# Kernel tuning notes

Measured on AMD Instinct MI355X. Metric: run time of the kernel, lower is better.

## Reference

```python
import jax, jax.numpy as jnp
import numpy as np

N_REGS, R_BIT, N_OPS, FLIP = 8, 16, 16, 2

def bit2dec(bits):
    # little-endian soft bits -> decimal: sum_k b_k * 2^k
    k = jnp.arange(bits.shape[-1], dtype=bits.dtype)
    return jnp.sum(bits * jnp.exp2(k), axis=-1)

def addr_w(idx, n):
    # differentiable soft one-hot over n slots (linear interpolation kernel)
    grid = jnp.arange(n, dtype=idx.dtype)
    return jnp.maximum(1.0 - jnp.abs(idx[..., None] - grid), 0.0)

def setup_inputs():
    key = jax.random.key(0)
    ks = jax.random.split(key, 12)
    B, H, I, L = 8192, 512, 1024, 16
    return dict(
        z_hidden=jax.random.normal(ks[0], (B, H), jnp.float32),
        P_op=jax.random.uniform(ks[1], (B, L, 4), dtype=jnp.float32),
        P_dst=jax.random.uniform(ks[2], (B, L, 3), dtype=jnp.float32),
        P_src1=jax.random.uniform(ks[3], (B, L, 3), dtype=jnp.float32),
        P_src2=jax.random.uniform(ks[4], (B, L, 3), dtype=jnp.float32),
        P_imm=jax.random.uniform(ks[5], (B, L, 3), dtype=jnp.float32),
        Proglen=jax.random.uniform(ks[6], (B, 4), dtype=jnp.float32),
        group_num=16,
        W1=jax.random.normal(ks[7], (H, I), jnp.float32) / np.sqrt(H).astype(np.float32),
        b1=jnp.zeros((I,), jnp.float32),
        WR=jax.random.normal(ks[8], (I, N_REGS * R_BIT), jnp.float32) / np.sqrt(I).astype(np.float32),
        bR=jnp.zeros((N_REGS * R_BIT,), jnp.float32),
        Wt=jax.random.normal(ks[9], (I, 1), jnp.float32) / np.sqrt(I).astype(np.float32),
        bt=jnp.zeros((1,), jnp.float32),
        W_r2h=jax.random.normal(ks[10], (N_REGS, H), jnp.float32) / np.sqrt(N_REGS).astype(np.float32),
        b_r2h=jnp.zeros((H,), jnp.float32),
        ln_g=jnp.ones((H,), jnp.float32),
        ln_b=jnp.zeros((H,), jnp.float32),
    )

def reference(z_hidden, P_op, P_dst, P_src1, P_src2, P_imm, Proglen, group_num,
              W1, b1, WR, bR, Wt, bt, W_r2h, b_r2h, ln_g, ln_b):
    B, L, G = z_hidden.shape[0], P_op.shape[1], group_num
    # ---- Augmentation_Layer: MLP head -> R soft-bits + threshold ----
    h = jax.nn.relu(z_hidden @ W1 + b1)
    R_bits = jax.nn.sigmoid(h @ WR + bR).reshape(B, N_REGS, R_BIT)
    threshold = jax.nn.sigmoid(h @ Wt + bt)                 # [B,1]
    # ---- GroupSample.generate4R: flip FLIP random R-bits per candidate (cand 0 = original) ----
    idx = jax.random.randint(jax.random.key(42), (B, G, FLIP), 0, N_REGS * R_BIT)
    mask = jnp.clip(jax.nn.one_hot(idx, N_REGS * R_BIT, dtype=jnp.float32).sum(-2), 0.0, 1.0)
    mask = mask.at[:, 0].set(0.0).reshape(B, G, N_REGS, R_BIT)
    Rb = R_bits[:, None]                                    # [B,1,n_regs,r_bit]
    R = bit2dec(Rb + mask * (1.0 - 2.0 * Rb))               # [B,G,n_regs] decimals
    M = jnp.zeros_like(R)
    prog_len = jnp.broadcast_to(bit2dec(Proglen)[:, None], (B, G))
    dec = lambda x: bit2dec(x).T                            # [L,B]
    prog = (dec(P_op), dec(P_dst), dec(P_src1), dec(P_src2), dec(P_imm),
            jnp.arange(L, dtype=jnp.float32))

    # ---- MultiInterpreter: differentiable soft register machine ----
    def step(carry, xs):
        R, M = carry
        op_t, dst_t, s1_t, s2_t, imm_t, t = xs
        bc = lambda v: jnp.broadcast_to(v[:, None], (B, G))
        op_t, dst_t, s1_t, s2_t, imm_t = map(bc, (op_t, dst_t, s1_t, s2_t, imm_t))
        active = jnp.clip(prog_len - t, 0.0, 1.0)           # halt mask [B,G]
        w_d = addr_w(dst_t, N_REGS)                         # [B,G,n_regs]
        w_1 = addr_w(s1_t, N_REGS)
        w_2 = addr_w(s2_t, N_REGS)
        w_op = addr_w(op_t, N_OPS)                          # [B,G,16]
        r1 = jnp.sum(w_1 * R, -1); r2 = jnp.sum(w_2 * R, -1)
        m1 = jnp.sum(w_1 * M, -1); old = jnp.sum(w_d * R, -1)
        results = jnp.stack([
            old,                       # 0 NOP
            r1 + r2,                   # 1 ADD
            r1 - r2,                   # 2 SUB
            r1 * r2 / 65536.0,         # 3 MUL (scaled by 2^r_bit)
            r1,                        # 4 MOV
            imm_t,                     # 5 LOADI
            r1 + imm_t,                # 6 ADDI
            jnp.maximum(r1, r2),       # 7 MAX
            jnp.minimum(r1, r2),       # 8 MIN
            -r1,                       # 9 NEG
            0.5 * r1,                  # 10 SHR
            r2,                        # 11 MOV2
            m1,                        # 12 LOAD M[src1]
            old,                       # 13 STORE (reg unchanged)
            jnp.abs(r1),               # 14 ABS
            old,                       # 15 NOP
        ], axis=-1)
        res = jnp.sum(w_op * results, -1)                   # [B,G]
        p_store = w_op[..., 13]
        R = R + active[..., None] * w_d * (res[..., None] - R)
        M = M + (active * p_store)[..., None] * w_d * (r1[..., None] - M)
        return (R, M), None

    (R, M), _ = jax.lax.scan(step, (R, M), prog)
    # ---- register2hidden + LayerNorm ----
    reg_hidden = R @ W_r2h + b_r2h                          # [B,G,H]
    mu = reg_hidden.mean(-1, keepdims=True)
    var = reg_hidden.var(-1, keepdims=True)
    reg_hidden = (reg_hidden - mu) * jax.lax.rsqrt(var + 1e-5) * ln_g + ln_b
    return reg_hidden, threshold
```

## Files before the change

kernel.cpp:

```cpp
#include <hip/hip_runtime.h>
#include <stdint.h>

typedef __attribute__((ext_vector_type(8))) short short8;
typedef __attribute__((ext_vector_type(4))) float f32x4;
typedef __attribute__((ext_vector_type(8))) unsigned short ushort8;
typedef __attribute__((ext_vector_type(4))) unsigned short ushort4v;

__device__ __forceinline__ unsigned short f2bf(float f) {
  uint32_t u = __float_as_uint(f);
  uint32_t r = (u + 0x7fffu + ((u >> 16) & 1u)) >> 16;
  return (unsigned short)r;
}
__device__ __forceinline__ float bf2f(unsigned short v) {
  return __uint_as_float(((uint32_t)v) << 16);
}

typedef __attribute__((address_space(1))) const unsigned int g_u32;
typedef __attribute__((address_space(3))) unsigned int l_u32;
__device__ __forceinline__ void gl_lds16(const void* g, void* l) {
  __builtin_amdgcn_global_load_lds((g_u32*)g, (l_u32*)l, 16, 0, 0);
}

__device__ __forceinline__ uint32_t rotl32(uint32_t v, int d) { return (v << d) | (v >> (32 - d)); }

__device__ __forceinline__ void threefry2x32(uint32_t k0, uint32_t k1, uint32_t& x0, uint32_t& x1) {
  const uint32_t ks2 = k0 ^ k1 ^ 0x1BD11BDAu;
  x0 += k0; x1 += k1;
  x0 += x1; x1 = rotl32(x1, 13); x1 ^= x0;
  x0 += x1; x1 = rotl32(x1, 15); x1 ^= x0;
  x0 += x1; x1 = rotl32(x1, 26); x1 ^= x0;
  x0 += x1; x1 = rotl32(x1, 6);  x1 ^= x0;
  x0 += k1; x1 += ks2 + 1u;
  x0 += x1; x1 = rotl32(x1, 17); x1 ^= x0;
  x0 += x1; x1 = rotl32(x1, 29); x1 ^= x0;
  x0 += x1; x1 = rotl32(x1, 16); x1 ^= x0;
  x0 += x1; x1 = rotl32(x1, 24); x1 ^= x0;
  x0 += ks2; x1 += k0 + 2u;
  x0 += x1; x1 = rotl32(x1, 13); x1 ^= x0;
  x0 += x1; x1 = rotl32(x1, 15); x1 ^= x0;
  x0 += x1; x1 = rotl32(x1, 26); x1 ^= x0;
  x0 += x1; x1 = rotl32(x1, 6);  x1 ^= x0;
  x0 += k0; x1 += k1 + 3u;
  x0 += x1; x1 = rotl32(x1, 17); x1 ^= x0;
  x0 += x1; x1 = rotl32(x1, 29); x1 ^= x0;
  x0 += x1; x1 = rotl32(x1, 16); x1 ^= x0;
  x0 += x1; x1 = rotl32(x1, 24); x1 ^= x0;
  x0 += k1; x1 += ks2 + 4u;
  x0 += x1; x1 = rotl32(x1, 13); x1 ^= x0;
  x0 += x1; x1 = rotl32(x1, 15); x1 ^= x0;
  x0 += x1; x1 = rotl32(x1, 26); x1 ^= x0;
  x0 += x1; x1 = rotl32(x1, 6);  x1 ^= x0;
  x0 += ks2; x1 += k0 + 5u;
}

__global__ __launch_bounds__(256) void prep_kernel(const float* __restrict__ z,
                                                   unsigned short* __restrict__ zb, int n8,
                                                   const float* __restrict__ W1,
                                                   const float* __restrict__ WR,
                                                   unsigned short* __restrict__ W1t,
                                                   unsigned short* __restrict__ WRt,
                                                   const float* __restrict__ P_op,
                                                   const float* __restrict__ P_dst,
                                                   const float* __restrict__ P_s1,
                                                   const float* __restrict__ P_s2,
                                                   const float* __restrict__ P_imm,
                                                   const float* __restrict__ Plen,
                                                   float* __restrict__ prog,
                                                   float* __restrict__ plen, int BT) {
  __shared__ float t[32][33];
  const int tid = threadIdx.x;
  const int bx = blockIdx.x;
  if (bx < 2048) {
    const int i = bx * 256 + tid;
    if (i >= n8) return;
    const float4 a = reinterpret_cast<const float4*>(z)[i * 2];
    const float4 b = reinterpret_cast<const float4*>(z)[i * 2 + 1];
    ushort8 u;
    u[0] = f2bf(a.x); u[1] = f2bf(a.y); u[2] = f2bf(a.z); u[3] = f2bf(a.w);
    u[4] = f2bf(b.x); u[5] = f2bf(b.y); u[6] = f2bf(b.z); u[7] = f2bf(b.w);
    reinterpret_cast<ushort8*>(zb)[i] = u;
  } else if (bx < 2688) {
    const int b = bx - 2048;
    const float* src; unsigned short* dst; int N, K, k0, n0;
    if (b < 512) {
      src = W1; dst = W1t; N = 1024; K = 512;
      k0 = (b & 15) * 32; n0 = (b >> 4) * 32;
    } else {
      const int b2 = b - 512;
      src = WR; dst = WRt; N = 128; K = 1024;
      k0 = (b2 & 31) * 32; n0 = (b2 >> 5) * 32;
    }
    {
      const int row = tid >> 3, c4 = (tid & 7) * 4;
      const float4 v = *reinterpret_cast<const float4*>(&src[(size_t)(k0 + row) * N + n0 + c4]);
      t[row][c4] = v.x; t[row][c4 + 1] = v.y; t[row][c4 + 2] = v.z; t[row][c4 + 3] = v.w;
    }
    __syncthreads();
    {
      const int n = tid >> 3, k4 = (tid & 7) * 4;
      ushort4v o;
      o.x = f2bf(t[k4 + 0][n]); o.y = f2bf(t[k4 + 1][n]);
      o.z = f2bf(t[k4 + 2][n]); o.w = f2bf(t[k4 + 3][n]);
      *reinterpret_cast<ushort4v*>(&dst[(size_t)(n0 + n) * K + k0 + k4]) = o;
    }
  } else {
    const int i = (bx - 2688) * 256 + tid;
    if (i >= BT) return;
    const float* po = P_op + (size_t)i * 4;
    const float op = po[0] + 2.f * po[1] + 4.f * po[2] + 8.f * po[3];
    const float* pd = P_dst + (size_t)i * 3;
    const float dv = pd[0] + 2.f * pd[1] + 4.f * pd[2];
    const float* p1 = P_s1 + (size_t)i * 3;
    const float s1v = p1[0] + 2.f * p1[1] + 4.f * p1[2];
    const float* p2 = P_s2 + (size_t)i * 3;
    const float s2v = p2[0] + 2.f * p2[1] + 4.f * p2[2];
    const float* pi = P_imm + (size_t)i * 3;
    const float imv = pi[0] + 2.f * pi[1] + 4.f * pi[2];
    float* o = prog + (size_t)i * 5;
    o[0] = op; o[1] = dv; o[2] = s1v; o[3] = s2v; o[4] = imv;
    if ((i & 15) == 0) {
      const int b = i >> 4;
      const float* pl = Plen + (size_t)b * 4;
      plen[b] = pl[0] + 2.f * pl[1] + 4.f * pl[2] + 8.f * pl[3];
    }
  }
}

__global__ __launch_bounds__(256) void gemm_fused(const unsigned short* __restrict__ zb,
                                                  const unsigned short* __restrict__ W1t,
                                                  const float* __restrict__ b1,
                                                  const unsigned short* __restrict__ WRt,
                                                  const float* __restrict__ Wt,
                                                  float* __restrict__ part,
                                                  float* __restrict__ thr_part, int B) {
  __shared__ __align__(16) char smem[34816];
  unsigned short* AsF = (unsigned short*)smem;
  unsigned short* BsF = (unsigned short*)(smem + 16384);
  auto H2 = reinterpret_cast<unsigned short (*)[136]>(smem);

  const int tid = threadIdx.x;
  const int lane = tid & 63, wave = tid >> 6;
  const int wm = wave >> 1, wn = wave & 1;
  const int bx = blockIdx.x, bm = blockIdx.y * 128, bn = bx * 128;

  f32x4 acc[4][4];
#pragma unroll
  for (int i = 0; i < 4; ++i)
#pragma unroll
    for (int j = 0; j < 4; ++j) acc[i][j] = (f32x4)0.f;

  const int fr = lane & 15, kc = (lane >> 4) * 8;
  const int lr = (lane >> 4) * 4, lc = lane & 15;
  const int lrow = lane >> 3, slot = lane & 7;
  const int sslot = (slot ^ lrow) << 3;
  const int fx = fr & 7;
  const int cbase = lane >> 4;

  for (int k0 = 0; k0 < 512; k0 += 64) {
#pragma unroll
    for (int i = 0; i < 4; ++i) {
      const int r0 = wave * 32 + i * 8;
      gl_lds16(&zb[(size_t)(bm + r0 + lrow) * 512 + k0 + sslot], &AsF[r0 * 64]);
    }
#pragma unroll
    for (int i = 0; i < 4; ++i) {
      const int r0 = wave * 32 + i * 8;
      gl_lds16(&W1t[(size_t)(bn + r0 + lrow) * 512 + k0 + sslot], &BsF[r0 * 64]);
    }
    __syncthreads();
#pragma unroll
    for (int s = 0; s < 2; ++s) {
      short8 af[4], bfv[4];
#pragma unroll
      for (int f = 0; f < 4; ++f) {
        const int row = wm * 64 + f * 16 + fr;
        const int c = s * 4 + cbase;
        af[f] = *reinterpret_cast<const short8*>(&AsF[row * 64 + ((c ^ fx) << 3)]);
      }
#pragma unroll
      for (int f = 0; f < 4; ++f) {
        const int row = wn * 64 + f * 16 + fr;
        const int c = s * 4 + cbase;
        bfv[f] = *reinterpret_cast<const short8*>(&BsF[row * 64 + ((c ^ fx) << 3)]);
      }
#pragma unroll
      for (int fm = 0; fm < 4; ++fm)
#pragma unroll
        for (int fn = 0; fn < 4; ++fn)
          acc[fm][fn] = __builtin_amdgcn_mfma_f32_16x16x32_bf16(af[fm], bfv[fn], acc[fm][fn], 0, 0, 0);
    }
    __syncthreads();
  }

#pragma unroll
  for (int fn = 0; fn < 4; ++fn) {
    const int col_l = wn * 64 + fn * 16 + lc;
    const float bv = b1[bn + col_l];
#pragma unroll
    for (int fm = 0; fm < 4; ++fm) {
      const int row_l0 = wm * 64 + fm * 16 + lr;
#pragma unroll
      for (int r = 0; r < 4; ++r)
        H2[row_l0 + r][col_l] = f2bf(fmaxf(acc[fm][fn][r] + bv, 0.f));
    }
  }
  __syncthreads();

  {
    const int row = tid >> 1, half = tid & 1;
    const unsigned short* hp = &H2[row][half * 64];
    const float* wp = &Wt[bn + half * 64];
    float s = 0.f;
#pragma unroll
    for (int j = 0; j < 8; ++j) {
      const ushort8 a = *reinterpret_cast<const ushort8*>(hp + j * 8);
      const float4 w0 = *reinterpret_cast<const float4*>(wp + j * 8);
      const float4 w1 = *reinterpret_cast<const float4*>(wp + j * 8 + 4);
      s += bf2f(a[0]) * w0.x + bf2f(a[1]) * w0.y + bf2f(a[2]) * w0.z + bf2f(a[3]) * w0.w;
      s += bf2f(a[4]) * w1.x + bf2f(a[5]) * w1.y + bf2f(a[6]) * w1.z + bf2f(a[7]) * w1.w;
    }
    s += __shfl_xor(s, 1);
    if (half == 0) thr_part[(size_t)bx * B + bm + row] = s;
  }

  f32x4 acc2[4][4];
#pragma unroll
  for (int i = 0; i < 4; ++i)
#pragma unroll
    for (int j = 0; j < 4; ++j) acc2[i][j] = (f32x4)0.f;

#pragma unroll
  for (int ks = 0; ks < 4; ++ks) {
    short8 af2[4], bf2v[4];
#pragma unroll
    for (int fm = 0; fm < 4; ++fm)
      af2[fm] = *reinterpret_cast<const short8*>(&H2[wm * 64 + fm * 16 + fr][ks * 32 + kc]);
#pragma unroll
    for (int fn = 0; fn < 4; ++fn)
      bf2v[fn] = *reinterpret_cast<const short8*>(
          &WRt[(size_t)(wn * 64 + fn * 16 + fr) * 1024 + bn + ks * 32 + kc]);
#pragma unroll
    for (int fm = 0; fm < 4; ++fm)
#pragma unroll
      for (int fn = 0; fn < 4; ++fn)
        acc2[fm][fn] = __builtin_amdgcn_mfma_f32_16x16x32_bf16(af2[fm], bf2v[fn], acc2[fm][fn], 0, 0, 0);
  }

  float* pp = part + (size_t)bx * B * 128;
#pragma unroll
  for (int fn = 0; fn < 4; ++fn) {
    const int col = wn * 64 + fn * 16 + lc;
#pragma unroll
    for (int fm = 0; fm < 4; ++fm) {
      const int row0 = bm + wm * 64 + fm * 16 + lr;
#pragma unroll
      for (int r = 0; r < 4; ++r)
        pp[(size_t)(row0 + r) * 128 + col] = acc2[fm][fn][r];
    }
  }
}

__global__ __launch_bounds__(256) void scan2_kernel(const float* __restrict__ part,
                                                    const float* __restrict__ bR,
                                                    const float* __restrict__ thr_part,
                                                    const float* __restrict__ bt,
                                                    const float* __restrict__ prog,
                                                    const float* __restrict__ plen,
                                                    float* __restrict__ Rfinal,
                                                    float* __restrict__ thr_out, int B) {
  __shared__ float s_bits[16][128];
  __shared__ float s_prog[16][80];
  __shared__ float s_plen[16];
  const int tid = threadIdx.x;
  const int b0 = blockIdx.x * 16;
#pragma unroll
  for (int j = 0; j < 8; ++j) {
    const int f = tid + 256 * j;
    const int lb = f >> 7, c = f & 127;
    float s = part[(size_t)(b0 + lb) * 128 + c];
#pragma unroll
    for (int sl = 1; sl < 8; ++sl)
      s += part[(size_t)sl * B * 128 + (size_t)(b0 + lb) * 128 + c];
    s_bits[lb][c] = 1.f / (1.f + expf(-(s + bR[c])));
  }
#pragma unroll
  for (int j = 0; j < 5; ++j) {
    const int f = tid + 256 * j;
    s_prog[f / 80][f % 80] = prog[(size_t)b0 * 80 + f];
  }
  if (tid < 16) {
    s_plen[tid] = plen[b0 + tid];
    float s = thr_part[b0 + tid];
#pragma unroll
    for (int sl = 1; sl < 8; ++sl) s += thr_part[(size_t)sl * B + b0 + tid];
    thr_out[b0 + tid] = 1.f / (1.f + expf(-(s + bt[0])));
  }
  __syncthreads();

  const int lb = tid >> 4, g = tid & 15;
  const int bg = (b0 + lb) * 16 + g;

  uint32_t k2a, k2b;
  { uint32_t x0 = 0u, x1 = 1u; threefry2x32(0u, 42u, x0, x1); k2a = x0; k2b = x1; }
  uint32_t p0, p1;
  {
    uint32_t x0 = 0u, x1 = (uint32_t)bg * 2u;
    threefry2x32(k2a, k2b, x0, x1);
    p0 = (x0 ^ x1) & 127u;
  }
  {
    uint32_t x0 = 0u, x1 = (uint32_t)bg * 2u + 1u;
    threefry2x32(k2a, k2b, x0, x1);
    p1 = (x0 ^ x1) & 127u;
  }

  float R[8], M[8];
#pragma unroll
  for (int r = 0; r < 8; ++r) {
    float a = 0.f;
#pragma unroll
    for (int bit = 0; bit < 16; ++bit) {
      const int pos = r * 16 + bit;
      float v = s_bits[lb][pos];
      const bool flip = (g != 0) && ((int)p0 == pos || (int)p1 == pos);
      v = flip ? 1.0f - v : v;
      a = fmaf(v, (float)(1 << bit), a);
    }
    R[r] = a;
    M[r] = 0.f;
  }

  const float pl = s_plen[lb];
  for (int t = 0; t < 16; ++t) {
    const float op = s_prog[lb][t * 5 + 0];
    const float dst = s_prog[lb][t * 5 + 1];
    const float sa = s_prog[lb][t * 5 + 2];
    const float sb = s_prog[lb][t * 5 + 3];
    const float imm = s_prog[lb][t * 5 + 4];
    const float active = fminf(fmaxf(pl - (float)t, 0.f), 1.f);
    float r1 = 0.f, r2 = 0.f, m1 = 0.f, old = 0.f;
    float wd[8];
#pragma unroll
    for (int i = 0; i < 8; ++i) {
      const float w1 = fmaxf(1.f - fabsf(sa - (float)i), 0.f);
      const float w2 = fmaxf(1.f - fabsf(sb - (float)i), 0.f);
      wd[i] = fmaxf(1.f - fabsf(dst - (float)i), 0.f);
      r1 = fmaf(w1, R[i], r1);
      r2 = fmaf(w2, R[i], r2);
      m1 = fmaf(w1, M[i], m1);
      old = fmaf(wd[i], R[i], old);
    }
    float results[16];
    results[0] = old;               results[1] = r1 + r2;
    results[2] = r1 - r2;           results[3] = r1 * r2 * (1.f / 65536.f);
    results[4] = r1;                results[5] = imm;
    results[6] = r1 + imm;          results[7] = fmaxf(r1, r2);
    results[8] = fminf(r1, r2);     results[9] = -r1;
    results[10] = 0.5f * r1;        results[11] = r2;
    results[12] = m1;               results[13] = old;
    results[14] = fabsf(r1);        results[15] = old;
    float res = 0.f;
    const float pstore = fmaxf(1.f - fabsf(op - 13.f), 0.f);
#pragma unroll
    for (int o = 0; o < 16; ++o) res = fmaf(fmaxf(1.f - fabsf(op - (float)o), 0.f), results[o], res);
#pragma unroll
    for (int i = 0; i < 8; ++i) {
      R[i] = fmaf(active * wd[i], res - R[i], R[i]);
      M[i] = fmaf(active * pstore * wd[i], r1 - M[i], M[i]);
    }
  }

  float* outp = Rfinal + (size_t)bg * 8;
#pragma unroll
  for (int r = 0; r < 8; ++r) outp[r] = R[r];
}

__global__ __launch_bounds__(256) void final_expand2(const float* __restrict__ Rf,
                                                     const float* __restrict__ W,
                                                     const float* __restrict__ bias,
                                                     const float* __restrict__ gam,
                                                     const float* __restrict__ bet,
                                                     float* __restrict__ out, int rowsPerWave) {
  const int lane = threadIdx.x & 63;
  const int w = blockIdx.x * 4 + (threadIdx.x >> 6);
  const int h0 = lane * 8;

  float wreg[8][8];
#pragma unroll
  for (int reg = 0; reg < 8; ++reg) {
    const float4 wa = *reinterpret_cast<const float4*>(&W[reg * 512 + h0]);
    const float4 wb = *reinterpret_cast<const float4*>(&W[reg * 512 + h0 + 4]);
    wreg[reg][0] = wa.x; wreg[reg][1] = wa.y; wreg[reg][2] = wa.z; wreg[reg][3] = wa.w;
    wreg[reg][4] = wb.x; wreg[reg][5] = wb.y; wreg[reg][6] = wb.z; wreg[reg][7] = wb.w;
  }
  float bi[8], ga[8], be[8];
  {
    const float4 a = *reinterpret_cast<const float4*>(&bias[h0]);
    const float4 b = *reinterpret_cast<const float4*>(&bias[h0 + 4]);
    bi[0] = a.x; bi[1] = a.y; bi[2] = a.z; bi[3] = a.w; bi[4] = b.x; bi[5] = b.y; bi[6] = b.z; bi[7] = b.w;
    const float4 c = *reinterpret_cast<const float4*>(&gam[h0]);
    const float4 d = *reinterpret_cast<const float4*>(&gam[h0 + 4]);
    ga[0] = c.x; ga[1] = c.y; ga[2] = c.z; ga[3] = c.w; ga[4] = d.x; ga[5] = d.y; ga[6] = d.z; ga[7] = d.w;
    const float4 e = *reinterpret_cast<const float4*>(&bet[h0]);
    const float4 f = *reinterpret_cast<const float4*>(&bet[h0 + 4]);
    be[0] = e.x; be[1] = e.y; be[2] = e.z; be[3] = e.w; be[4] = f.x; be[5] = f.y; be[6] = f.z; be[7] = f.w;
  }

  const int r0 = w * rowsPerWave;
  for (int i = 0; i < rowsPerWave; ++i) {
    const int row = r0 + i;
    const float4 ra = *reinterpret_cast<const float4*>(&Rf[(size_t)row * 8]);
    const float4 rb = *reinterpret_cast<const float4*>(&Rf[(size_t)row * 8 + 4]);
    const float r[8] = {ra.x, ra.y, ra.z, ra.w, rb.x, rb.y, rb.z, rb.w};
    float x[8];
#pragma unroll
    for (int j = 0; j < 8; ++j) x[j] = bi[j];
#pragma unroll
    for (int reg = 0; reg < 8; ++reg)
#pragma unroll
      for (int j = 0; j < 8; ++j) x[j] = fmaf(r[reg], wreg[reg][j], x[j]);
    float s1 = 0.f, s2 = 0.f;
#pragma unroll
    for (int j = 0; j < 8; ++j) { s1 += x[j]; s2 = fmaf(x[j], x[j], s2); }
#pragma unroll
    for (int off = 32; off; off >>= 1) { s1 += __shfl_xor(s1, off); s2 += __shfl_xor(s2, off); }
    const float mean = s1 * (1.f / 512.f);
    const float var = s2 * (1.f / 512.f) - mean * mean;
    const float inv = rsqrtf(var + 1e-5f);
    float y[8];
#pragma unroll
    for (int j = 0; j < 8; ++j) y[j] = (x[j] - mean) * inv * ga[j] + be[j];
    float* dst = out + (size_t)row * 512 + h0;
    *reinterpret_cast<float4*>(dst) = make_float4(y[0], y[1], y[2], y[3]);
    *reinterpret_cast<float4*>(dst + 4) = make_float4(y[4], y[5], y[6], y[7]);
  }
}

extern "C" void kernel_launch(void* const* d_in, const int* in_sizes, int n_in,
                              void* d_out, int out_size, void* d_ws, size_t ws_size,
                              hipStream_t stream) {
  const float* z    = (const float*)d_in[0];
  const float* P_op = (const float*)d_in[1];
  const float* P_dst= (const float*)d_in[2];
  const float* P_s1 = (const float*)d_in[3];
  const float* P_s2 = (const float*)d_in[4];
  const float* P_imm= (const float*)d_in[5];
  const float* Plen = (const float*)d_in[6];
  const float* W1   = (const float*)d_in[8];
  const float* b1   = (const float*)d_in[9];
  const float* WR   = (const float*)d_in[10];
  const float* bR   = (const float*)d_in[11];
  const float* Wt   = (const float*)d_in[12];
  const float* bt   = (const float*)d_in[13];
  const float* W_r2h= (const float*)d_in[14];
  const float* b_r2h= (const float*)d_in[15];
  const float* ln_g = (const float*)d_in[16];
  const float* ln_b = (const float*)d_in[17];

  const int B = in_sizes[0] / 512;
  float* out = (float*)d_out;
  float* part    = out + (size_t)(1 << 25);
  float* thr_out = out + (size_t)B * 16 * 512;

  float* ws = (float*)d_ws;
  float* prog   = ws;
  float* plen   = prog + (size_t)B * 80;
  float* Rfinal = plen + B;
  float* thr_part = Rfinal + (size_t)B * 128;
  unsigned short* W1t = (unsigned short*)(thr_part + (size_t)8 * B);
  unsigned short* WRt = W1t + (size_t)1024 * 512;
  unsigned short* zb  = WRt + (size_t)128 * 1024;

  const dim3 blk(256);
  prep_kernel<<<dim3(3200), blk, 0, stream>>>(z, zb, B * 512 / 8, W1, WR, W1t, WRt,
                                              P_op, P_dst, P_s1, P_s2, P_imm, Plen,
                                              prog, plen, B * 16);
  gemm_fused<<<dim3(8, B / 128), blk, 0, stream>>>(zb, W1t, b1, WRt, Wt, part, thr_part, B);
  scan2_kernel<<<dim3(B / 16), blk, 0, stream>>>(part, bR, thr_part, bt, prog, plen, Rfinal,
                                                 thr_out, B);
  final_expand2<<<dim3(B * 16 / 4 / 32), blk, 0, stream>>>(Rfinal, W_r2h, b_r2h, ln_g, ln_b, out,
                                                           32);
}
```

Measured before the change: 112.7 us.

## Move WR/threshold GEMM into scan kernel and fuse register2hidden LayerNorm

The first GEMM now writes the full bf16 hidden activation to workspace instead of per-N-tile partial WR products. The scan kernel loads 16 hidden rows into LDS and computes the WR GEMM and threshold dot product itself, removing the 8-way partial-sum buffers and their reduction. When workspace is large enough, it also runs the register-to-hidden projection and LayerNorm in the same kernel, dropping the final launch and the Rfinal round trip. The cost is a large LDS footprint per block, which lowers occupancy, and a serial K=1024 MFMA loop per wave that rereads WRt from global memory in every block.

```diff
diff --git a/kernel.cpp b/kernel.cpp
--- a/kernel.cpp
+++ b/kernel.cpp
@@ -126,13 +126,10 @@
   }
 }
 
-__global__ __launch_bounds__(256) void gemm_fused(const unsigned short* __restrict__ zb,
-                                                  const unsigned short* __restrict__ W1t,
-                                                  const float* __restrict__ b1,
-                                                  const unsigned short* __restrict__ WRt,
-                                                  const float* __restrict__ Wt,
-                                                  float* __restrict__ part,
-                                                  float* __restrict__ thr_part, int B) {
+__global__ __launch_bounds__(256) void gemm1_kernel(const unsigned short* __restrict__ zb,
+                                                    const unsigned short* __restrict__ W1t,
+                                                    const float* __restrict__ b1,
+                                                    unsigned short* __restrict__ h) {
   __shared__ __align__(16) char smem[34816];
   unsigned short* AsF = (unsigned short*)smem;
   unsigned short* BsF = (unsigned short*)(smem + 16384);
@@ -141,7 +138,7 @@
   const int tid = threadIdx.x;
   const int lane = tid & 63, wave = tid >> 6;
   const int wm = wave >> 1, wn = wave & 1;
-  const int bx = blockIdx.x, bm = blockIdx.y * 128, bn = bx * 128;
+  const int bm = blockIdx.y * 128, bn = blockIdx.x * 128;
 
   f32x4 acc[4][4];
 #pragma unroll
@@ -149,7 +146,7 @@
 #pragma unroll
     for (int j = 0; j < 4; ++j) acc[i][j] = (f32x4)0.f;
 
-  const int fr = lane & 15, kc = (lane >> 4) * 8;
+  const int fr = lane & 15;
   const int lr = (lane >> 4) * 4, lc = lane & 15;
   const int lrow = lane >> 3, slot = lane & 7;
   const int sslot = (slot ^ lrow) << 3;
@@ -205,95 +202,90 @@
     }
   }
   __syncthreads();
-
-  {
-    const int row = tid >> 1, half = tid & 1;
-    const unsigned short* hp = &H2[row][half * 64];
-    const float* wp = &Wt[bn + half * 64];
-    float s = 0.f;
-#pragma unroll
-    for (int j = 0; j < 8; ++j) {
-      const ushort8 a = *reinterpret_cast<const ushort8*>(hp + j * 8);
-      const float4 w0 = *reinterpret_cast<const float4*>(wp + j * 8);
-      const float4 w1 = *reinterpret_cast<const float4*>(wp + j * 8 + 4);
-      s += bf2f(a[0]) * w0.x + bf2f(a[1]) * w0.y + bf2f(a[2]) * w0.z + bf2f(a[3]) * w0.w;
-      s += bf2f(a[4]) * w1.x + bf2f(a[5]) * w1.y + bf2f(a[6]) * w1.z + bf2f(a[7]) * w1.w;
-    }
-    s += __shfl_xor(s, 1);
-    if (half == 0) thr_part[(size_t)bx * B + bm + row] = s;
-  }
-
-  f32x4 acc2[4][4];
-#pragma unroll
-  for (int i = 0; i < 4; ++i)
-#pragma unroll
-    for (int j = 0; j < 4; ++j) acc2[i][j] = (f32x4)0.f;
-
-#pragma unroll
-  for (int ks = 0; ks < 4; ++ks) {
-    short8 af2[4], bf2v[4];
-#pragma unroll
-    for (int fm = 0; fm < 4; ++fm)
-      af2[fm] = *reinterpret_cast<const short8*>(&H2[wm * 64 + fm * 16 + fr][ks * 32 + kc]);
-#pragma unroll
-    for (int fn = 0; fn < 4; ++fn)
-      bf2v[fn] = *reinterpret_cast<const short8*>(
-          &WRt[(size_t)(wn * 64 + fn * 16 + fr) * 1024 + bn + ks * 32 + kc]);
-#pragma unroll
-    for (int fm = 0; fm < 4; ++fm)
-#pragma unroll
-      for (int fn = 0; fn < 4; ++fn)
-        acc2[fm][fn] = __builtin_amdgcn_mfma_f32_16x16x32_bf16(af2[fm], bf2v[fn], acc2[fm][fn], 0, 0, 0);
-  }
-
-  float* pp = part + (size_t)bx * B * 128;
-#pragma unroll
-  for (int fn = 0; fn < 4; ++fn) {
-    const int col = wn * 64 + fn * 16 + lc;
-#pragma unroll
-    for (int fm = 0; fm < 4; ++fm) {
-      const int row0 = bm + wm * 64 + fm * 16 + lr;
-#pragma unroll
-      for (int r = 0; r < 4; ++r)
-        pp[(size_t)(row0 + r) * 128 + col] = acc2[fm][fn][r];
-    }
-  }
-}
-
-__global__ __launch_bounds__(256) void scan2_kernel(const float* __restrict__ part,
+  {
+    const int row = tid >> 1, c0 = (tid & 1) * 64;
+    unsigned short* hp = &h[(size_t)(bm + row) * 1024 + bn + c0];
+#pragma unroll
+    for (int j = 0; j < 8; ++j)
+      *reinterpret_cast<ushort8*>(hp + j * 8) = *reinterpret_cast<const ushort8*>(&H2[row][c0 + j * 8]);
+  }
+}
+
+template <bool FUSE>
+__global__ __launch_bounds__(256) void scan3_kernel(const unsigned short* __restrict__ h,
+                                                    const unsigned short* __restrict__ WRt,
                                                     const float* __restrict__ bR,
-                                                    const float* __restrict__ thr_part,
+                                                    const float* __restrict__ Wt,
                                                     const float* __restrict__ bt,
                                                     const float* __restrict__ prog,
                                                     const float* __restrict__ plen,
+                                                    const float* __restrict__ W,
+                                                    const float* __restrict__ bias,
+                                                    const float* __restrict__ gam,
+                                                    const float* __restrict__ bet,
                                                     float* __restrict__ Rfinal,
-                                                    float* __restrict__ thr_out, int B) {
-  __shared__ float s_bits[16][128];
-  __shared__ float s_prog[16][80];
-  __shared__ float s_plen[16];
+                                                    float* __restrict__ thr_out,
+                                                    float* __restrict__ out) {
+  __shared__ __align__(16) char arena[46400];
+  auto h_lds = reinterpret_cast<unsigned short (*)[1032]>(arena);
+  float* sb = reinterpret_cast<float*>(arena + 33024);
+  float* sp = reinterpret_cast<float*>(arena + 41216);
+  float* spl = reinterpret_cast<float*>(arena + 46336);
+
   const int tid = threadIdx.x;
+  const int lane = tid & 63, wave = tid >> 6;
   const int b0 = blockIdx.x * 16;
+
 #pragma unroll
   for (int j = 0; j < 8; ++j) {
-    const int f = tid + 256 * j;
-    const int lb = f >> 7, c = f & 127;
-    float s = part[(size_t)(b0 + lb) * 128 + c];
-#pragma unroll
-    for (int sl = 1; sl < 8; ++sl)
-      s += part[(size_t)sl * B * 128 + (size_t)(b0 + lb) * 128 + c];
-    s_bits[lb][c] = 1.f / (1.f + expf(-(s + bR[c])));
+    const int idx = tid + 256 * j;
+    const int row = idx >> 7, seg = idx & 127;
+    *reinterpret_cast<ushort8*>(&h_lds[row][seg * 8]) =
+        *reinterpret_cast<const ushort8*>(&h[(size_t)(b0 + row) * 1024 + seg * 8]);
   }
 #pragma unroll
   for (int j = 0; j < 5; ++j) {
     const int f = tid + 256 * j;
-    s_prog[f / 80][f % 80] = prog[(size_t)b0 * 80 + f];
-  }
-  if (tid < 16) {
-    s_plen[tid] = plen[b0 + tid];
-    float s = thr_part[b0 + tid];
-#pragma unroll
-    for (int sl = 1; sl < 8; ++sl) s += thr_part[(size_t)sl * B + b0 + tid];
-    thr_out[b0 + tid] = 1.f / (1.f + expf(-(s + bt[0])));
+    sp[f] = prog[(size_t)b0 * 80 + f];
+  }
+  if (tid < 16) spl[tid] = plen[b0 + tid];
+  __syncthreads();
+
+  {
+    f32x4 acc0 = (f32x4)0.f, acc1 = (f32x4)0.f;
+    const int fr = lane & 15, khi = (lane >> 4) * 8;
+    const int n0 = wave * 32;
+#pragma unroll
+    for (int k0 = 0; k0 < 1024; k0 += 32) {
+      const short8 af = *reinterpret_cast<const short8*>(&h_lds[fr][k0 + khi]);
+      const short8 bf0 = *reinterpret_cast<const short8*>(&WRt[(size_t)(n0 + fr) * 1024 + k0 + khi]);
+      const short8 bf1 = *reinterpret_cast<const short8*>(&WRt[(size_t)(n0 + 16 + fr) * 1024 + k0 + khi]);
+      acc0 = __builtin_amdgcn_mfma_f32_16x16x32_bf16(af, bf0, acc0, 0, 0, 0);
+      acc1 = __builtin_amdgcn_mfma_f32_16x16x32_bf16(af, bf1, acc1, 0, 0, 0);
+    }
+    const int col0 = n0 + (lane & 15), col1 = n0 + 16 + (lane & 15);
+    const float bb0 = bR[col0], bb1 = bR[col1];
+#pragma unroll
+    for (int r = 0; r < 4; ++r) {
+      const int row = (lane >> 4) * 4 + r;
+      sb[row * 128 + col0] = 1.f / (1.f + expf(-(acc0[r] + bb0)));
+      sb[row * 128 + col1] = 1.f / (1.f + expf(-(acc1[r] + bb1)));
+    }
+  }
+
+  {
+    const int lb = tid >> 4, sg = (tid & 15) * 64;
+    float s = 0.f;
+#pragma unroll
+    for (int j = 0; j < 8; ++j) {
+      const ushort8 a = *reinterpret_cast<const ushort8*>(&h_lds[lb][sg + j * 8]);
+      const float4 w0 = *reinterpret_cast<const float4*>(&Wt[sg + j * 8]);
+      const float4 w1 = *reinterpret_cast<const float4*>(&Wt[sg + j * 8 + 4]);
+      s += bf2f(a[0]) * w0.x + bf2f(a[1]) * w0.y + bf2f(a[2]) * w0.z + bf2f(a[3]) * w0.w;
+      s += bf2f(a[4]) * w1.x + bf2f(a[5]) * w1.y + bf2f(a[6]) * w1.z + bf2f(a[7]) * w1.w;
+    }
+    s += __shfl_xor(s, 1); s += __shfl_xor(s, 2); s += __shfl_xor(s, 4); s += __shfl_xor(s, 8);
+    if ((tid & 15) == 0) thr_out[b0 + lb] = 1.f / (1.f + expf(-(s + bt[0])));
   }
   __syncthreads();
 
@@ -321,7 +313,7 @@
 #pragma unroll
     for (int bit = 0; bit < 16; ++bit) {
       const int pos = r * 16 + bit;
-      float v = s_bits[lb][pos];
+      float v = sb[lb * 128 + pos];
       const bool flip = (g != 0) && ((int)p0 == pos || (int)p1 == pos);
       v = flip ? 1.0f - v : v;
       a = fmaf(v, (float)(1 << bit), a);
@@ -330,20 +322,20 @@
     M[r] = 0.f;
   }
 
-  const float pl = s_plen[lb];
+  const float pl = spl[lb];
   for (int t = 0; t < 16; ++t) {
-    const float op = s_prog[lb][t * 5 + 0];
-    const float dst = s_prog[lb][t * 5 + 1];
-    const float sa = s_prog[lb][t * 5 + 2];
-    const float sb = s_prog[lb][t * 5 + 3];
-    const float imm = s_prog[lb][t * 5 + 4];
+    const float op = sp[lb * 80 + t * 5 + 0];
+    const float dst = sp[lb * 80 + t * 5 + 1];
+    const float sa = sp[lb * 80 + t * 5 + 2];
+    const float sbv = sp[lb * 80 + t * 5 + 3];
+    const float imm = sp[lb * 80 + t * 5 + 4];
     const float active = fminf(fmaxf(pl - (float)t, 0.f), 1.f);
     float r1 = 0.f, r2 = 0.f, m1 = 0.f, old = 0.f;
     float wd[8];
 #pragma unroll
     for (int i = 0; i < 8; ++i) {
       const float w1 = fmaxf(1.f - fabsf(sa - (float)i), 0.f);
-      const float w2 = fmaxf(1.f - fabsf(sb - (float)i), 0.f);
+      const float w2 = fmaxf(1.f - fabsf(sbv - (float)i), 0.f);
       wd[i] = fmaxf(1.f - fabsf(dst - (float)i), 0.f);
       r1 = fmaf(w1, R[i], r1);
       r2 = fmaf(w2, R[i], r2);
@@ -370,9 +362,69 @@
     }
   }
 
-  float* outp = Rfinal + (size_t)bg * 8;
-#pragma unroll
-  for (int r = 0; r < 8; ++r) outp[r] = R[r];
+  if (!FUSE) {
+    float* outp = Rfinal + (size_t)bg * 8;
+#pragma unroll
+    for (int r = 0; r < 8; ++r) outp[r] = R[r];
+    return;
+  }
+
+  __syncthreads();
+  float* Rs = sb;
+#pragma unroll
+  for (int r = 0; r < 8; ++r) Rs[tid * 8 + r] = R[r];
+  __syncthreads();
+
+  const int h0 = lane * 8;
+  float wreg[8][8];
+#pragma unroll
+  for (int reg = 0; reg < 8; ++reg) {
+    const float4 wa = *reinterpret_cast<const float4*>(&W[reg * 512 + h0]);
+    const float4 wb = *reinterpret_cast<const float4*>(&W[reg * 512 + h0 + 4]);
+    wreg[reg][0] = wa.x; wreg[reg][1] = wa.y; wreg[reg][2] = wa.z; wreg[reg][3] = wa.w;
+    wreg[reg][4] = wb.x; wreg[reg][5] = wb.y; wreg[reg][6] = wb.z; wreg[reg][7] = wb.w;
+  }
+  float bi[8], ga[8], be[8];
+  {
+    const float4 a = *reinterpret_cast<const float4*>(&bias[h0]);
+    const float4 b = *reinterpret_cast<const float4*>(&bias[h0 + 4]);
+    bi[0] = a.x; bi[1] = a.y; bi[2] = a.z; bi[3] = a.w; bi[4] = b.x; bi[5] = b.y; bi[6] = b.z; bi[7] = b.w;
+    const float4 c = *reinterpret_cast<const float4*>(&gam[h0]);
+    const float4 d = *reinterpret_cast<const float4*>(&gam[h0 + 4]);
+    ga[0] = c.x; ga[1] = c.y; ga[2] = c.z; ga[3] = c.w; ga[4] = d.x; ga[5] = d.y; ga[6] = d.z; ga[7] = d.w;
+    const float4 e = *reinterpret_cast<const float4*>(&bet[h0]);
+    const float4 f = *reinterpret_cast<const float4*>(&bet[h0 + 4]);
+    be[0] = e.x; be[1] = e.y; be[2] = e.z; be[3] = e.w; be[4] = f.x; be[5] = f.y; be[6] = f.z; be[7] = f.w;
+  }
+
+  const size_t rbase = (size_t)b0 * 16;
+  for (int i = 0; i < 64; ++i) {
+    const int rl = wave * 64 + i;
+    const float4 ra = *reinterpret_cast<const float4*>(&Rs[rl * 8]);
+    const float4 rb = *reinterpret_cast<const float4*>(&Rs[rl * 8 + 4]);
+    const float rr[8] = {ra.x, ra.y, ra.z, ra.w, rb.x, rb.y, rb.z, rb.w};
+    float x[8];
+#pragma unroll
+    for (int j = 0; j < 8; ++j) x[j] = bi[j];
+#pragma unroll
+    for (int reg = 0; reg < 8; ++reg)
+#pragma unroll
+      for (int j = 0; j < 8; ++j) x[j] = fmaf(rr[reg], wreg[reg][j], x[j]);
+    float s1 = 0.f, s2 = 0.f;
+#pragma unroll
+    for (int j = 0; j < 8; ++j) { s1 += x[j]; s2 = fmaf(x[j], x[j], s2); }
+#pragma unroll
+    for (int off = 32; off; off >>= 1) { s1 += __shfl_xor(s1, off); s2 += __shfl_xor(s2, off); }
+    const float mean = s1 * (1.f / 512.f);
+    const float var = s2 * (1.f / 512.f) - mean * mean;
+    const float inv = rsqrtf(var + 1e-5f);
+    float y[8];
+#pragma unroll
+    for (int j = 0; j < 8; ++j) y[j] = (x[j] - mean) * inv * ga[j] + be[j];
+    float* dst = out + (rbase + rl) * 512 + h0;
+    *reinterpret_cast<float4*>(dst) = make_float4(y[0], y[1], y[2], y[3]);
+    *reinterpret_cast<float4*>(dst + 4) = make_float4(y[4], y[5], y[6], y[7]);
+  }
 }
 
 __global__ __launch_bounds__(256) void final_expand2(const float* __restrict__ Rf,
@@ -459,25 +511,35 @@
 
   const int B = in_sizes[0] / 512;
   float* out = (float*)d_out;
-  float* part    = out + (size_t)(1 << 25);
   float* thr_out = out + (size_t)B * 16 * 512;
 
   float* ws = (float*)d_ws;
   float* prog   = ws;
   float* plen   = prog + (size_t)B * 80;
   float* Rfinal = plen + B;
-  float* thr_part = Rfinal + (size_t)B * 128;
-  unsigned short* W1t = (unsigned short*)(thr_part + (size_t)8 * B);
+  unsigned short* W1t = (unsigned short*)(Rfinal + (size_t)B * 128);
   unsigned short* WRt = W1t + (size_t)1024 * 512;
   unsigned short* zb  = WRt + (size_t)128 * 1024;
+  unsigned short* h_ws = zb + (size_t)B * 512;
+
+  const size_t need = (size_t)((char*)(h_ws + (size_t)B * 1024) - (char*)d_ws);
+  const bool fuse = ws_size >= need;
+  unsigned short* h = fuse ? h_ws : (unsigned short*)(out + (size_t)(1 << 25));
 
   const dim3 blk(256);
   prep_kernel<<<dim3(3200), blk, 0, stream>>>(z, zb, B * 512 / 8, W1, WR, W1t, WRt,
                                               P_op, P_dst, P_s1, P_s2, P_imm, Plen,
                                               prog, plen, B * 16);
-  gemm_fused<<<dim3(8, B / 128), blk, 0, stream>>>(zb, W1t, b1, WRt, Wt, part, thr_part, B);
-  scan2_kernel<<<dim3(B / 16), blk, 0, stream>>>(part, bR, thr_part, bt, prog, plen, Rfinal,
-                                                 thr_out, B);
-  final_expand2<<<dim3(B * 16 / 4 / 32), blk, 0, stream>>>(Rfinal, W_r2h, b_r2h, ln_g, ln_b, out,
-                                                           32);
-}
+  gemm1_kernel<<<dim3(8, B / 128), blk, 0, stream>>>(zb, W1t, b1, h);
+  if (fuse) {
+    scan3_kernel<true><<<dim3(B / 16), blk, 0, stream>>>(h, WRt, bR, Wt, bt, prog, plen,
+                                                         W_r2h, b_r2h, ln_g, ln_b,
+                                                         Rfinal, thr_out, out);
+  } else {
+    scan3_kernel<false><<<dim3(B / 16), blk, 0, stream>>>(h, WRt, bR, Wt, bt, prog, plen,
+                                                          W_r2h, b_r2h, ln_g, ln_b,
+                                                          Rfinal, thr_out, out);
+    final_expand2<<<dim3(B * 16 / 4 / 32), blk, 0, stream>>>(Rfinal, W_r2h, b_r2h, ln_g, ln_b,
+                                                             out, 32);
+  }
+}
```

New measurement: 117.0 us. 1.04x slower.
